# Kernel tuning notes

Hardware: AMD Instinct MI355X
Metric: run time of the kernel (lower is better)

The kernel has to match this reference:

```python
import jax, jax.numpy as jnp
import numpy as np

N = 1024   # num nodes (assets)
F = 128    # node feature dim (node_dim)
M = 256    # memory_dim (scorer hidden)
E = 8      # edge_dim
BN_EPS = 1e-5


def setup_inputs() -> dict:
    key = jax.random.key(0)
    ks = jax.random.split(key, 6)
    x = jax.random.normal(ks[0], (N, F), dtype=jnp.float32)
    ctx = jax.random.uniform(ks[1], (4,), dtype=jnp.float32)  # [crisis_prob, ttc/30, urgency, confidence]
    W1 = jax.random.normal(ks[2], (M, 2 * F + 4), dtype=jnp.float32) * 0.05
    b1 = jnp.zeros((M,), jnp.float32)
    gamma = jnp.ones((M,), jnp.float32)
    beta = jnp.zeros((M,), jnp.float32)
    run_mean = jnp.zeros((M,), jnp.float32)
    run_var = jnp.ones((M,), jnp.float32)
    W2 = jax.random.normal(ks[3], (E, M), dtype=jnp.float32) * 0.05
    b2 = jnp.zeros((E,), jnp.float32)
    W3 = jax.random.normal(ks[4], (1, E), dtype=jnp.float32) * 0.05
    b3 = jnp.zeros((1,), jnp.float32)
    return {"x": x, "ctx": ctx, "W1": W1, "b1": b1, "gamma": gamma, "beta": beta,
            "run_mean": run_mean, "run_var": run_var, "W2": W2, "b2": b2, "W3": W3, "b3": b3}


def reference(x, ctx, W1, b1, gamma, beta, run_mean, run_var, W2, b2, W3, b3):
    # All unordered pairs i<j (static shapes); original loops over stressed pairs only,
    # we score all pairs and expose the stressed/threshold filter as a boolean mask.
    ii, jj = jnp.triu_indices(N, k=1)  # each [P], P = N*(N-1)/2

    # First linear decomposed: W1 @ [x_i; x_j; ctx] = A x_i + B x_j + (C ctx + b1)
    pa = x @ W1[:, :F].T          # [N, M]
    pb = x @ W1[:, F:2 * F].T     # [N, M]
    cterm = ctx @ W1[:, 2 * F:].T + b1  # [M]

    h = jax.nn.relu(pa[ii] + pb[jj] + cterm)                           # [P, M]
    h = gamma * (h - run_mean) * jax.lax.rsqrt(run_var + BN_EPS) + beta  # eval-mode BatchNorm1d
    h = jax.nn.relu(h @ W2.T + b2)                                     # [P, E]
    scores = jax.nn.sigmoid(h @ W3.T + b3)[:, 0]                       # [P]

    # Stressed-node selection: std over feature dim > mean std (torch unbiased std)
    stress = x.std(axis=1, ddof=1)
    stressed = stress > stress.mean()
    edge_mask = (scores > 0.5) & stressed[ii] & stressed[jj]           # [P] bool
    return scores, edge_mask
```

## Files before the change

kernel.cpp:

```cpp
#include <hip/hip_runtime.h>
#include <math.h>

#define N_NODES 1024
#define F_DIM   128
#define M_DIM   256
#define E_DIM   8
#define P_PAIRS 523776
#define NBLK    1056
#define APITCH  33

typedef float v2f __attribute__((ext_vector_type(2)));

__global__ __launch_bounds__(256) void kA(const float* __restrict__ x,
                                          const float* __restrict__ ctx,
                                          const float* __restrict__ W1,
                                          const float* __restrict__ b1,
                                          const float* __restrict__ gamma,
                                          const float* __restrict__ beta,
                                          const float* __restrict__ rmean,
                                          const float* __restrict__ rvar,
                                          const float* __restrict__ W2,
                                          const float* __restrict__ b2,
                                          float* __restrict__ pa,
                                          float* __restrict__ pb,
                                          float* __restrict__ stress,
                                          float* __restrict__ w2ft,
                                          float* __restrict__ b2f) {
  const int t = threadIdx.x;

  if (blockIdx.x == 256) {
    __shared__ float bnbs[256];
    const float s   = gamma[t] / sqrtf(rvar[t] + 1e-5f);
    bnbs[t] = beta[t] - s * rmean[t];
    #pragma unroll
    for (int e = 0; e < 8; ++e) w2ft[t * 8 + e] = W2[e * 256 + t] * s;
    __syncthreads();
    const int wv = t >> 6, lane = t & 63;
    #pragma unroll
    for (int r = 0; r < 2; ++r) {
      const int e = wv * 2 + r;
      float acc = 0.f;
      #pragma unroll
      for (int k = 0; k < 4; ++k) acc += W2[e * 256 + lane + 64 * k] * bnbs[lane + 64 * k];
      #pragma unroll
      for (int m = 32; m > 0; m >>= 1) acc += __shfl_xor(acc, m, 64);
      if (lane == 0) b2f[e] = acc + b2[e];
    }
    return;
  }

  __shared__ float xv[4][128];
  const int n0 = blockIdx.x * 4;
  if (t < 128) {
    ((float4*)&xv[0][0])[t] = ((const float4*)(x + (size_t)n0 * F_DIM))[t];
  }
  __syncthreads();

  {
    const int wv = t >> 6, lane = t & 63;
    const float a = xv[wv][lane], b = xv[wv][lane + 64];
    float sum = a + b;
    #pragma unroll
    for (int m = 32; m > 0; m >>= 1) sum += __shfl_xor(sum, m, 64);
    const float mean = sum * (1.0f / 128.0f);
    const float d0 = a - mean, d1 = b - mean;
    float ss = d0 * d0 + d1 * d1;
    #pragma unroll
    for (int m = 32; m > 0; m >>= 1) ss += __shfl_xor(ss, m, 64);
    if (lane == 0) stress[n0 + wv] = sqrtf(ss * (1.0f / 127.0f));
  }

  const float4* wrow = (const float4*)(W1 + (size_t)t * 260);
  float accA[4] = {0.f, 0.f, 0.f, 0.f};
  float accB[4] = {0.f, 0.f, 0.f, 0.f};
  #pragma unroll 8
  for (int k4 = 0; k4 < 32; ++k4) {
    const float4 wa = wrow[k4];
    const float4 wb = wrow[32 + k4];
    #pragma unroll
    for (int nn = 0; nn < 4; ++nn) {
      const float4 xf = ((const float4*)&xv[nn][0])[k4];
      accA[nn] = fmaf(xf.w, wa.w, fmaf(xf.z, wa.z, fmaf(xf.y, wa.y, fmaf(xf.x, wa.x, accA[nn]))));
      accB[nn] = fmaf(xf.w, wb.w, fmaf(xf.z, wb.z, fmaf(xf.y, wb.y, fmaf(xf.x, wb.x, accB[nn]))));
    }
  }
  const float c0 = ctx[0], c1 = ctx[1], c2 = ctx[2], c3 = ctx[3];
  const float* rowt = W1 + (size_t)t * 260 + 256;
  const float ctv = b1[t] + c0 * rowt[0] + c1 * rowt[1] + c2 * rowt[2] + c3 * rowt[3];
  #pragma unroll
  for (int nn = 0; nn < 4; ++nn) {
    pa[(size_t)(n0 + nn) * M_DIM + t] = accA[nn] + ctv;
    pb[(size_t)(n0 + nn) * M_DIM + t] = accB[nn];
  }
}

__global__ __launch_bounds__(256, 4) void kC(const float* __restrict__ pa,
                                             const float* __restrict__ pb,
                                             const float* __restrict__ w2ft,
                                             const float* __restrict__ b2f,
                                             const float* __restrict__ W3,
                                             const float* __restrict__ b3,
                                             const float* __restrict__ stress,
                                             float* __restrict__ out) {
  __shared__ float4 a4[16 * APITCH];
  __shared__ float4 b4[32 * APITCH];
  const int t = threadIdx.x;

  const int p = blockIdx.x;
  int tj = (int)((sqrtf(4.0f * (float)p + 1.0f) - 1.0f) * 0.5f);
  while ((tj + 1) * (tj + 2) <= p) ++tj;
  while (tj * (tj + 1) > p) --tj;
  const int si = p - tj * (tj + 1);
  const int i0 = si * 16, j0 = tj * 32;

  float ssum = 0.f;
  {
    const int lane = t & 63;
    #pragma unroll
    for (int k = 0; k < 16; ++k) ssum += stress[lane + 64 * k];
    #pragma unroll
    for (int m = 32; m > 0; m >>= 1) ssum += __shfl_xor(ssum, m, 64);
  }
  const float smean = ssum * (1.0f / 1024.0f);

  const int jx = t & 15;
  const int iy = t >> 4;
  v2f accJ[8];
  #pragma unroll
  for (int e = 0; e < 8; ++e) accJ[e] = (v2f){0.f, 0.f};

  const float4* pa4 = (const float4*)pa;
  const float4* pb4 = (const float4*)pb;
  const double* wdp = (const double*)w2ft;

  float4 rg[6];

  #pragma unroll
  for (int q = 0; q < 6; ++q) {
    if (q < 2) {
      const int d = q * 256 + t, r = d >> 5, c = d & 31;
      rg[q] = pa4[(size_t)(i0 + r) * 64 + c];
    } else {
      const int d2 = (q - 2) * 256 + t, r = d2 >> 5, c = d2 & 31;
      rg[q] = pb4[(size_t)(j0 + r) * 64 + c];
    }
  }
  #pragma unroll
  for (int q = 0; q < 6; ++q) {
    if (q < 2) {
      const int d = q * 256 + t, r = d >> 5, c = d & 31;
      a4[r * APITCH + c] = rg[q];
    } else {
      const int d2 = (q - 2) * 256 + t, r = d2 >> 5, c = d2 & 31;
      b4[r * APITCH + c] = rg[q];
    }
  }
  __syncthreads();

  #pragma unroll
  for (int q = 0; q < 6; ++q) {
    if (q < 2) {
      const int d = q * 256 + t, r = d >> 5, c = d & 31;
      rg[q] = pa4[(size_t)(i0 + r) * 64 + 32 + c];
    } else {
      const int d2 = (q - 2) * 256 + t, r = d2 >> 5, c = d2 & 31;
      rg[q] = pb4[(size_t)(j0 + r) * 64 + 32 + c];
    }
  }

  const float4* aRow  = a4 + iy * APITCH;
  const float4* bRow0 = b4 + jx * APITCH;
  const float4* bRow1 = b4 + (jx + 16) * APITCH;

  auto computeChunk = [&](int cw) {
    #pragma unroll 4
    for (int m4 = 0; m4 < 32; ++m4) {
      const float4 a0 = aRow[m4];
      const float4 b0 = bRow0[m4];
      const float4 b1 = bRow1[m4];
      const double* wr = wdp + (size_t)(cw + m4) * 16;

      const float* a0f = (const float*)&a0;
      const float* b0f = (const float*)&b0;
      const float* b1f = (const float*)&b1;
      #pragma unroll
      for (int mm = 0; mm < 4; ++mm) {
        v2f r;
        r.x = fmaxf(a0f[mm] + b0f[mm], 0.f);
        r.y = fmaxf(a0f[mm] + b1f[mm], 0.f);
        #pragma unroll
        for (int k = 0; k < 4; ++k) {
          const double wp = wr[mm * 4 + k];
          asm("v_pk_fma_f32 %0, %1, %2, %0 op_sel:[0,0,0] op_sel_hi:[0,1,1]"
              : "+v"(accJ[2 * k]) : "s"(wp), "v"(r));
          asm("v_pk_fma_f32 %0, %1, %2, %0 op_sel:[1,0,0] op_sel_hi:[1,1,1]"
              : "+v"(accJ[2 * k + 1]) : "s"(wp), "v"(r));
        }
      }
    }
  };

  computeChunk(0);
  __syncthreads();
  #pragma unroll
  for (int q = 0; q < 6; ++q) {
    if (q < 2) {
      const int d = q * 256 + t, r = d >> 5, c = d & 31;
      a4[r * APITCH + c] = rg[q];
    } else {
      const int d2 = (q - 2) * 256 + t, r = d2 >> 5, c = d2 & 31;
      b4[r * APITCH + c] = rg[q];
    }
  }
  __syncthreads();
  computeChunk(32);

  float w3v[8], b2v[8];
  #pragma unroll
  for (int e = 0; e < 8; ++e) { w3v[e] = W3[e]; b2v[e] = b2f[e]; }
  const float b3v = b3[0];
  const int i = i0 + iy;
  #pragma unroll
  for (int jb = 0; jb < 2; ++jb) {
    const int j = j0 + jx + jb * 16;
    if (i < j) {
      float logit = b3v;
      #pragma unroll
      for (int e = 0; e < 8; ++e) {
        const float av = jb ? accJ[e].y : accJ[e].x;
        const float h2 = fmaxf(av + b2v[e], 0.f);
        logit = fmaf(w3v[e], h2, logit);
      }
      const float score = 1.0f / (1.0f + expf(-logit));
      const int idx = i * 1023 - (i * (i - 1)) / 2 + (j - i - 1);
      out[idx] = score;
      const bool mk = (score > 0.5f) && (stress[i] > smean) && (stress[j] > smean);
      out[P_PAIRS + idx] = mk ? 1.0f : 0.0f;
    }
  }
}

extern "C" void kernel_launch(void* const* d_in, const int* in_sizes, int n_in,
                              void* d_out, int out_size, void* d_ws, size_t ws_size,
                              hipStream_t stream) {
  const float* x     = (const float*)d_in[0];
  const float* ctx   = (const float*)d_in[1];
  const float* W1    = (const float*)d_in[2];
  const float* b1    = (const float*)d_in[3];
  const float* gamma = (const float*)d_in[4];
  const float* beta  = (const float*)d_in[5];
  const float* rmean = (const float*)d_in[6];
  const float* rvar  = (const float*)d_in[7];
  const float* W2    = (const float*)d_in[8];
  const float* b2    = (const float*)d_in[9];
  const float* W3    = (const float*)d_in[10];
  const float* b3    = (const float*)d_in[11];
  float* out = (float*)d_out;

  float* ws     = (float*)d_ws;
  float* pa     = ws;
  float* pb     = pa + 262144;
  float* w2ft   = pb + 262144;
  float* b2f    = w2ft + 2048;
  float* stress = b2f + 8;

  hipLaunchKernelGGL(kA, dim3(257), dim3(256), 0, stream, x, ctx, W1, b1, gamma, beta,
                     rmean, rvar, W2, b2, pa, pb, stress, w2ft, b2f);
  hipLaunchKernelGGL(kC, dim3(NBLK), dim3(256), 0, stream, pa, pb, w2ft, b2f,
                     W3, b3, stress, out);
}
```

Measured before the change: 127.8 us.

## Shrink pair tile to 16x16 per block and raise occupancy

The pair-scoring kernel now covers a 16x16 (i,j) tile per block instead of 16x32, so there are 2080 triangular blocks instead of 1056. Each thread computes one pair with a packed FMA over all 8 edge outputs rather than two pairs. Launch bounds go to 8 waves per SIMD and the register-staged prefetch of the second half is dropped for a simple load-sync-compute loop. The aim is lower register pressure, higher occupancy and less wasted work on diagonal tiles. In exchange each block does less compute per shared-memory load and loses the overlap of global loads with compute.

```diff
diff --git a/kernel.cpp b/kernel.cpp
--- a/kernel.cpp
+++ b/kernel.cpp
@@ -6,7 +6,7 @@
 #define M_DIM   256
 #define E_DIM   8
 #define P_PAIRS 523776
-#define NBLK    1056
+#define NBLK    2080
 #define APITCH  33
 
 typedef float v2f __attribute__((ext_vector_type(2)));
@@ -94,7 +94,7 @@
   }
 }
 
-__global__ __launch_bounds__(256, 4) void kC(const float* __restrict__ pa,
+__global__ __launch_bounds__(256, 8) void kC(const float* __restrict__ pa,
                                              const float* __restrict__ pb,
                                              const float* __restrict__ w2ft,
                                              const float* __restrict__ b2f,
@@ -103,15 +103,15 @@
                                              const float* __restrict__ stress,
                                              float* __restrict__ out) {
   __shared__ float4 a4[16 * APITCH];
-  __shared__ float4 b4[32 * APITCH];
+  __shared__ float4 b4[16 * APITCH];
   const int t = threadIdx.x;
 
   const int p = blockIdx.x;
-  int tj = (int)((sqrtf(4.0f * (float)p + 1.0f) - 1.0f) * 0.5f);
-  while ((tj + 1) * (tj + 2) <= p) ++tj;
-  while (tj * (tj + 1) > p) --tj;
-  const int si = p - tj * (tj + 1);
-  const int i0 = si * 16, j0 = tj * 32;
+  int tj = (int)((sqrtf(8.0f * (float)p + 1.0f) - 1.0f) * 0.5f);
+  while ((tj + 1) * (tj + 2) / 2 <= p) ++tj;
+  while (tj * (tj + 1) / 2 > p) --tj;
+  const int ti = p - tj * (tj + 1) / 2;
+  const int i0 = ti * 16, j0 = tj * 16;
 
   float ssum = 0.f;
   {
@@ -125,118 +125,69 @@
 
   const int jx = t & 15;
   const int iy = t >> 4;
-  v2f accJ[8];
-  #pragma unroll
-  for (int e = 0; e < 8; ++e) accJ[e] = (v2f){0.f, 0.f};
+  v2f acc[4];
+  #pragma unroll
+  for (int k = 0; k < 4; ++k) acc[k] = (v2f){0.f, 0.f};
 
   const float4* pa4 = (const float4*)pa;
   const float4* pb4 = (const float4*)pb;
   const double* wdp = (const double*)w2ft;
 
-  float4 rg[6];
-
-  #pragma unroll
-  for (int q = 0; q < 6; ++q) {
-    if (q < 2) {
+  const float4* aRow = a4 + iy * APITCH;
+  const float4* bRow = b4 + jx * APITCH;
+
+  #pragma unroll
+  for (int cb = 0; cb < 2; ++cb) {
+    if (cb) __syncthreads();
+    #pragma unroll
+    for (int q = 0; q < 2; ++q) {
       const int d = q * 256 + t, r = d >> 5, c = d & 31;
-      rg[q] = pa4[(size_t)(i0 + r) * 64 + c];
-    } else {
-      const int d2 = (q - 2) * 256 + t, r = d2 >> 5, c = d2 & 31;
-      rg[q] = pb4[(size_t)(j0 + r) * 64 + c];
-    }
-  }
-  #pragma unroll
-  for (int q = 0; q < 6; ++q) {
-    if (q < 2) {
-      const int d = q * 256 + t, r = d >> 5, c = d & 31;
-      a4[r * APITCH + c] = rg[q];
-    } else {
-      const int d2 = (q - 2) * 256 + t, r = d2 >> 5, c = d2 & 31;
-      b4[r * APITCH + c] = rg[q];
-    }
-  }
-  __syncthreads();
-
-  #pragma unroll
-  for (int q = 0; q < 6; ++q) {
-    if (q < 2) {
-      const int d = q * 256 + t, r = d >> 5, c = d & 31;
-      rg[q] = pa4[(size_t)(i0 + r) * 64 + 32 + c];
-    } else {
-      const int d2 = (q - 2) * 256 + t, r = d2 >> 5, c = d2 & 31;
-      rg[q] = pb4[(size_t)(j0 + r) * 64 + 32 + c];
-    }
-  }
-
-  const float4* aRow  = a4 + iy * APITCH;
-  const float4* bRow0 = b4 + jx * APITCH;
-  const float4* bRow1 = b4 + (jx + 16) * APITCH;
-
-  auto computeChunk = [&](int cw) {
-    #pragma unroll 4
+      a4[r * APITCH + c] = pa4[(size_t)(i0 + r) * 64 + cb * 32 + c];
+      b4[r * APITCH + c] = pb4[(size_t)(j0 + r) * 64 + cb * 32 + c];
+    }
+    __syncthreads();
+
+    const int cw = cb * 32;
+    #pragma unroll 2
     for (int m4 = 0; m4 < 32; ++m4) {
-      const float4 a0 = aRow[m4];
-      const float4 b0 = bRow0[m4];
-      const float4 b1 = bRow1[m4];
+      const float4 A = aRow[m4];
+      const float4 B = bRow[m4];
       const double* wr = wdp + (size_t)(cw + m4) * 16;
-
-      const float* a0f = (const float*)&a0;
-      const float* b0f = (const float*)&b0;
-      const float* b1f = (const float*)&b1;
+      const float* Af = (const float*)&A;
+      const float* Bf = (const float*)&B;
       #pragma unroll
       for (int mm = 0; mm < 4; ++mm) {
-        v2f r;
-        r.x = fmaxf(a0f[mm] + b0f[mm], 0.f);
-        r.y = fmaxf(a0f[mm] + b1f[mm], 0.f);
+        const float r = fmaxf(Af[mm] + Bf[mm], 0.f);
+        const v2f rr = {r, r};
         #pragma unroll
         for (int k = 0; k < 4; ++k) {
           const double wp = wr[mm * 4 + k];
-          asm("v_pk_fma_f32 %0, %1, %2, %0 op_sel:[0,0,0] op_sel_hi:[0,1,1]"
-              : "+v"(accJ[2 * k]) : "s"(wp), "v"(r));
-          asm("v_pk_fma_f32 %0, %1, %2, %0 op_sel:[1,0,0] op_sel_hi:[1,1,1]"
-              : "+v"(accJ[2 * k + 1]) : "s"(wp), "v"(r));
+          asm("v_pk_fma_f32 %0, %1, %2, %0"
+              : "+v"(acc[k]) : "s"(wp), "v"(rr));
         }
       }
     }
-  };
-
-  computeChunk(0);
-  __syncthreads();
-  #pragma unroll
-  for (int q = 0; q < 6; ++q) {
-    if (q < 2) {
-      const int d = q * 256 + t, r = d >> 5, c = d & 31;
-      a4[r * APITCH + c] = rg[q];
-    } else {
-      const int d2 = (q - 2) * 256 + t, r = d2 >> 5, c = d2 & 31;
-      b4[r * APITCH + c] = rg[q];
-    }
-  }
-  __syncthreads();
-  computeChunk(32);
+  }
 
   float w3v[8], b2v[8];
   #pragma unroll
   for (int e = 0; e < 8; ++e) { w3v[e] = W3[e]; b2v[e] = b2f[e]; }
   const float b3v = b3[0];
   const int i = i0 + iy;
-  #pragma unroll
-  for (int jb = 0; jb < 2; ++jb) {
-    const int j = j0 + jx + jb * 16;
-    if (i < j) {
-      float logit = b3v;
-      #pragma unroll
-      for (int e = 0; e < 8; ++e) {
-        const float av = jb ? accJ[e].y : accJ[e].x;
-        const float h2 = fmaxf(av + b2v[e], 0.f);
-        logit = fmaf(w3v[e], h2, logit);
-      }
-      const float score = 1.0f / (1.0f + expf(-logit));
-      const int idx = i * 1023 - (i * (i - 1)) / 2 + (j - i - 1);
-      out[idx] = score;
-      const bool mk = (score > 0.5f) && (stress[i] > smean) && (stress[j] > smean);
-      out[P_PAIRS + idx] = mk ? 1.0f : 0.0f;
-    }
+  const int j = j0 + jx;
+  if (i < j) {
+    const float* af = (const float*)&acc[0];
+    float logit = b3v;
+    #pragma unroll
+    for (int e = 0; e < 8; ++e) {
+      const float h2 = fmaxf(af[e] + b2v[e], 0.f);
+      logit = fmaf(w3v[e], h2, logit);
+    }
+    const float score = 1.0f / (1.0f + expf(-logit));
+    const int idx = i * 1023 - (i * (i - 1)) / 2 + (j - i - 1);
+    out[idx] = score;
+    const bool mk = (score > 0.5f) && (stress[i] > smean) && (stress[j] > smean);
+    out[P_PAIRS + idx] = mk ? 1.0f : 0.0f;
   }
 }
 
```

Measured after the change: 123.8 us. 3.2% less time.

## Raise kC occupancy to 6 blocks and drop second-half register prefetch

Applied to the files above, without the earlier changes.

Raises the kC launch-bounds minimum to 6 blocks per CU. It stops prefetching the second half of the pa/pb tiles into registers during the first compute chunk and loads it only after that chunk finishes. It also issues the first-half global loads before the stress reduction and lowers the inner unroll from 4 to 2, all to cut VGPR use so more waves fit. In exchange, the second-half load latency is no longer hidden behind compute and is exposed between the two chunks, relying on the extra occupancy to cover it.

```diff
diff --git a/kernel.cpp b/kernel.cpp
--- a/kernel.cpp
+++ b/kernel.cpp
@@ -94,7 +94,7 @@
   }
 }
 
-__global__ __launch_bounds__(256, 4) void kC(const float* __restrict__ pa,
+__global__ __launch_bounds__(256, 6) void kC(const float* __restrict__ pa,
                                              const float* __restrict__ pb,
                                              const float* __restrict__ w2ft,
                                              const float* __restrict__ b2f,
@@ -113,6 +113,22 @@
   const int si = p - tj * (tj + 1);
   const int i0 = si * 16, j0 = tj * 32;
 
+  const float4* pa4 = (const float4*)pa;
+  const float4* pb4 = (const float4*)pb;
+  const double* wdp = (const double*)w2ft;
+
+  float4 rA[2], rB[4];
+  #pragma unroll
+  for (int q = 0; q < 2; ++q) {
+    const int d = q * 256 + t, r = d >> 5, c = d & 31;
+    rA[q] = pa4[(size_t)(i0 + r) * 64 + c];
+  }
+  #pragma unroll
+  for (int q = 0; q < 4; ++q) {
+    const int d = q * 256 + t, r = d >> 5, c = d & 31;
+    rB[q] = pb4[(size_t)(j0 + r) * 64 + c];
+  }
+
   float ssum = 0.f;
   {
     const int lane = t & 63;
@@ -123,78 +139,50 @@
   }
   const float smean = ssum * (1.0f / 1024.0f);
 
+  #pragma unroll
+  for (int q = 0; q < 2; ++q) {
+    const int d = q * 256 + t, r = d >> 5, c = d & 31;
+    a4[r * APITCH + c] = rA[q];
+  }
+  #pragma unroll
+  for (int q = 0; q < 4; ++q) {
+    const int d = q * 256 + t, r = d >> 5, c = d & 31;
+    b4[r * APITCH + c] = rB[q];
+  }
+  __syncthreads();
+
   const int jx = t & 15;
   const int iy = t >> 4;
-  v2f accJ[8];
-  #pragma unroll
-  for (int e = 0; e < 8; ++e) accJ[e] = (v2f){0.f, 0.f};
-
-  const float4* pa4 = (const float4*)pa;
-  const float4* pb4 = (const float4*)pb;
-  const double* wdp = (const double*)w2ft;
-
-  float4 rg[6];
-
-  #pragma unroll
-  for (int q = 0; q < 6; ++q) {
-    if (q < 2) {
-      const int d = q * 256 + t, r = d >> 5, c = d & 31;
-      rg[q] = pa4[(size_t)(i0 + r) * 64 + c];
-    } else {
-      const int d2 = (q - 2) * 256 + t, r = d2 >> 5, c = d2 & 31;
-      rg[q] = pb4[(size_t)(j0 + r) * 64 + c];
-    }
-  }
-  #pragma unroll
-  for (int q = 0; q < 6; ++q) {
-    if (q < 2) {
-      const int d = q * 256 + t, r = d >> 5, c = d & 31;
-      a4[r * APITCH + c] = rg[q];
-    } else {
-      const int d2 = (q - 2) * 256 + t, r = d2 >> 5, c = d2 & 31;
-      b4[r * APITCH + c] = rg[q];
-    }
-  }
-  __syncthreads();
-
-  #pragma unroll
-  for (int q = 0; q < 6; ++q) {
-    if (q < 2) {
-      const int d = q * 256 + t, r = d >> 5, c = d & 31;
-      rg[q] = pa4[(size_t)(i0 + r) * 64 + 32 + c];
-    } else {
-      const int d2 = (q - 2) * 256 + t, r = d2 >> 5, c = d2 & 31;
-      rg[q] = pb4[(size_t)(j0 + r) * 64 + 32 + c];
-    }
-  }
+  v2f acc[8];
+  #pragma unroll
+  for (int e = 0; e < 8; ++e) acc[e] = (v2f){0.f, 0.f};
 
   const float4* aRow  = a4 + iy * APITCH;
   const float4* bRow0 = b4 + jx * APITCH;
   const float4* bRow1 = b4 + (jx + 16) * APITCH;
 
   auto computeChunk = [&](int cw) {
-    #pragma unroll 4
+    #pragma unroll 2
     for (int m4 = 0; m4 < 32; ++m4) {
-      const float4 a0 = aRow[m4];
-      const float4 b0 = bRow0[m4];
-      const float4 b1 = bRow1[m4];
+      const float4 A  = aRow[m4];
+      const float4 B0 = bRow0[m4];
+      const float4 B1 = bRow1[m4];
       const double* wr = wdp + (size_t)(cw + m4) * 16;
-
-      const float* a0f = (const float*)&a0;
-      const float* b0f = (const float*)&b0;
-      const float* b1f = (const float*)&b1;
+      const float* Af  = (const float*)&A;
+      const float* B0f = (const float*)&B0;
+      const float* B1f = (const float*)&B1;
       #pragma unroll
       for (int mm = 0; mm < 4; ++mm) {
-        v2f r;
-        r.x = fmaxf(a0f[mm] + b0f[mm], 0.f);
-        r.y = fmaxf(a0f[mm] + b1f[mm], 0.f);
+        v2f R;
+        R.x = fmaxf(Af[mm] + B0f[mm], 0.f);
+        R.y = fmaxf(Af[mm] + B1f[mm], 0.f);
         #pragma unroll
         for (int k = 0; k < 4; ++k) {
           const double wp = wr[mm * 4 + k];
           asm("v_pk_fma_f32 %0, %1, %2, %0 op_sel:[0,0,0] op_sel_hi:[0,1,1]"
-              : "+v"(accJ[2 * k]) : "s"(wp), "v"(r));
+              : "+v"(acc[2 * k]) : "s"(wp), "v"(R));
           asm("v_pk_fma_f32 %0, %1, %2, %0 op_sel:[1,0,0] op_sel_hi:[1,1,1]"
-              : "+v"(accJ[2 * k + 1]) : "s"(wp), "v"(r));
+              : "+v"(acc[2 * k + 1]) : "s"(wp), "v"(R));
         }
       }
     }
@@ -202,17 +190,29 @@
 
   computeChunk(0);
   __syncthreads();
-  #pragma unroll
-  for (int q = 0; q < 6; ++q) {
-    if (q < 2) {
-      const int d = q * 256 + t, r = d >> 5, c = d & 31;
-      a4[r * APITCH + c] = rg[q];
-    } else {
-      const int d2 = (q - 2) * 256 + t, r = d2 >> 5, c = d2 & 31;
-      b4[r * APITCH + c] = rg[q];
-    }
-  }
-  __syncthreads();
+
+  #pragma unroll
+  for (int q = 0; q < 2; ++q) {
+    const int d = q * 256 + t, r = d >> 5, c = d & 31;
+    rA[q] = pa4[(size_t)(i0 + r) * 64 + 32 + c];
+  }
+  #pragma unroll
+  for (int q = 0; q < 4; ++q) {
+    const int d = q * 256 + t, r = d >> 5, c = d & 31;
+    rB[q] = pb4[(size_t)(j0 + r) * 64 + 32 + c];
+  }
+  #pragma unroll
+  for (int q = 0; q < 2; ++q) {
+    const int d = q * 256 + t, r = d >> 5, c = d & 31;
+    a4[r * APITCH + c] = rA[q];
+  }
+  #pragma unroll
+  for (int q = 0; q < 4; ++q) {
+    const int d = q * 256 + t, r = d >> 5, c = d & 31;
+    b4[r * APITCH + c] = rB[q];
+  }
+  __syncthreads();
+
   computeChunk(32);
 
   float w3v[8], b2v[8];
@@ -227,7 +227,7 @@
       float logit = b3v;
       #pragma unroll
       for (int e = 0; e < 8; ++e) {
-        const float av = jb ? accJ[e].y : accJ[e].x;
+        const float av = jb ? acc[e].y : acc[e].x;
         const float h2 = fmaxf(av + b2v[e], 0.f);
         logit = fmaf(w3v[e], h2, logit);
       }
```

Result: faster. 119.4 us (-6.6%).
